# Performance work log

Measured on AMD Instinct MI355X. Metric: run time of the kernel, lower is better.

## Reference

```python
import jax, jax.numpy as jnp
import numpy as np

B, S, K = 4, 2048, 8
N_NEURONS, N_BASIS, RANK = 64, 32, 8
D_MODEL, D_HID = 256, 1024


def setup_inputs() -> dict:
    key = jax.random.key(0)
    ks = jax.random.split(key, 10)
    x = jax.random.normal(ks[0], (B, S, D_MODEL), dtype=jnp.float32)
    neuron_idx = jax.random.randint(ks[1], (B, S, K), 0, N_NEURONS)
    w = jax.random.uniform(ks[2], (B, S, K), dtype=jnp.float32)
    neuron_weights = w / jnp.sum(w, axis=-1, keepdims=True)  # softmax-like routing weights
    neuron_recipes = jax.random.normal(ks[3], (N_NEURONS, N_BASIS), dtype=jnp.float32) * 0.5
    sc = 0.1
    basis_A1 = jax.random.normal(ks[4], (N_BASIS, 16, RANK, 8), dtype=jnp.float32) * sc
    basis_A2 = jax.random.normal(ks[5], (N_BASIS, RANK, 16, 8), dtype=jnp.float32) * sc
    basis_B1 = jax.random.normal(ks[6], (N_BASIS, 8, RANK, 32), dtype=jnp.float32) * sc
    basis_B2 = jax.random.normal(ks[7], (N_BASIS, RANK, 8, 32), dtype=jnp.float32) * sc
    w_down_w = jax.random.normal(ks[8], (D_HID, D_MODEL), dtype=jnp.float32) * (1.0 / np.sqrt(D_HID))
    w_down_b = jnp.zeros((D_MODEL,), dtype=jnp.float32)
    return {
        "x": x, "neuron_idx": neuron_idx, "neuron_weights": neuron_weights,
        "neuron_recipes": neuron_recipes,
        "basis_A1": basis_A1, "basis_A2": basis_A2,
        "basis_B1": basis_B1, "basis_B2": basis_B2,
        "w_down_w": w_down_w, "w_down_b": w_down_b,
    }


def reference(x, neuron_idx, neuron_weights, neuron_recipes,
              basis_A1, basis_A2, basis_B1, basis_B2, w_down_w, w_down_b):
    Bt, St, D = x.shape
    # --- routing: gather recipes of selected neurons, softmax, weighted-combine ---
    sel = neuron_recipes[neuron_idx]                       # [B,S,k,n_basis]
    sel = jax.nn.softmax(sel, axis=-1)
    wr = jnp.einsum('bskn,bsk->bsn', sel, neuron_weights)  # [B,S,n_basis]
    # --- build per-token TT cores from basis banks (get_neuron_tt_cores) ---
    cA1 = jnp.einsum('bsn,nirk->bsirk', wr, basis_A1)      # [B,S,16,r,8]
    cA2 = jnp.einsum('bsn,nrjl->bsrjl', wr, basis_A2)      # [B,S,r,16,8]
    cB1 = jnp.einsum('bsn,nirk->bsirk', wr, basis_B1)      # [B,S,8,r,32]
    cB2 = jnp.einsum('bsn,nrjl->bsrjl', wr, basis_B2)      # [B,S,r,8,32]
    # --- TT FFN: 256 -> 64 ---
    x_fold = x.reshape(Bt, St, 16, 16)
    temp = jnp.einsum('bsij,bsirk->bsjrk', x_fold, cA1)
    h = jnp.einsum('bsjrk,bsrjl->bskl', temp, cA2).reshape(Bt, St, 64)
    # --- TT FFN: 64 -> 1024 ---
    h_fold = h.reshape(Bt, St, 8, 8)
    temp = jnp.einsum('bsij,bsirk->bsjrk', h_fold, cB1)
    out = jnp.einsum('bsjrk,bsrjl->bskl', temp, cB2).reshape(Bt, St, D_HID)
    out = jax.nn.gelu(out, approximate=False)              # torch F.gelu default = exact erf
    return out @ w_down_w + w_down_b                       # [B,S,256]
```

## Files before the change

### kernel.cpp

```cpp
#include <hip/hip_runtime.h>
#include <math.h>


typedef unsigned short u16;
typedef __attribute__((ext_vector_type(8))) __bf16 bf16x8;
typedef __attribute__((ext_vector_type(4))) float f32x4;
union ABCast { float4 f; bf16x8 v; };
union BFBits { __bf16 b; u16 u; };
union Pack8 { u16 u[8]; float4 f; };

__device__ __forceinline__ float gelu_exact(float v) {
    return 0.5f * v * (1.0f + erff(v * 0.70710678118654752440f));
}
__device__ __forceinline__ u16 f2bf_bits(float f) { BFBits c; c.b = (__bf16)f; return c.u; }
__device__ __forceinline__ float bfbits2f(u16 u) { BFBits c; c.u = u; return (float)c.b; }

__global__ __launch_bounds__(64) void k_route(
    const int* __restrict__ nidx, const float* __restrict__ nw,
    const float* __restrict__ recipes, float* __restrict__ wr_out,
    u16* __restrict__ wrAh, u16* __restrict__ wrAl)
{
    const int t = blockIdx.x * 64 + threadIdx.x;
    float acc[32];
#pragma unroll
    for (int n = 0; n < 32; n++) acc[n] = 0.f;
#pragma unroll
    for (int k = 0; k < 8; k++) {
        const int   id = nidx[t * 8 + k];
        const float wk = nw[t * 8 + k];
        const float4* row = (const float4*)(recipes + id * 32);
        float v[32];
#pragma unroll
        for (int q = 0; q < 8; q++) {
            float4 f = row[q];
            v[q*4+0] = f.x; v[q*4+1] = f.y; v[q*4+2] = f.z; v[q*4+3] = f.w;
        }
        float m = v[0];
#pragma unroll
        for (int n = 1; n < 32; n++) m = fmaxf(m, v[n]);
        float s = 0.f;
#pragma unroll
        for (int n = 0; n < 32; n++) { float e = expf(v[n] - m); v[n] = e; s += e; }
        const float iv = wk / s;
#pragma unroll
        for (int n = 0; n < 32; n++) acc[n] += v[n] * iv;
    }
    float4* o = (float4*)(wr_out + t * 32);
#pragma unroll
    for (int q = 0; q < 8; q++)
        o[q] = make_float4(acc[q*4+0], acc[q*4+1], acc[q*4+2], acc[q*4+3]);

    const int tg16 = t >> 4, tl = t & 15;
#pragma unroll
    for (int c = 0; c < 4; c++) {
        Pack8 ph, pl;
#pragma unroll
        for (int e = 0; e < 8; e++) {
            const float v = acc[c*8 + e];
            const u16 hb = f2bf_bits(v);
            ph.u[e] = hb;
            pl.u[e] = f2bf_bits(v - bfbits2f(hb));
        }
        const int lane = c * 16 + tl;
        *(float4*)(wrAh + (tg16*64 + lane)*8) = ph.f;
        *(float4*)(wrAl + (tg16*64 + lane)*8) = pl.f;
    }
}

__global__ __launch_bounds__(512) void k_stageA(
    const float* __restrict__ x, const float* __restrict__ wr,
    const float* __restrict__ A1, const float* __restrict__ A2,
    float* __restrict__ h_out)
{
    __shared__ float ca[8 * 1024];
    __shared__ float tl[8 * 1088];
    const int tid = threadIdx.x;
    const int t0  = blockIdx.x * 8;
    {
        const int e2 = tid * 2;
        float2 c[8];
#pragma unroll
        for (int tt = 0; tt < 8; tt++) c[tt] = make_float2(0.f, 0.f);
#pragma unroll 4
        for (int n = 0; n < 32; n++) {
            const float2 a = *(const float2*)(A1 + n * 1024 + e2);
#pragma unroll
            for (int tt = 0; tt < 8; tt++) {
                const float s = wr[(t0 + tt) * 32 + n];
                c[tt].x += s * a.x; c[tt].y += s * a.y;
            }
        }
#pragma unroll
        for (int tt = 0; tt < 8; tt++) *(float2*)(ca + tt * 1024 + e2) = c[tt];
    }
    __syncthreads();
    {
        const int t = tid >> 6, g = tid & 63, j = g >> 2, eh = g & 3;
        float xr[16];
#pragma unroll
        for (int i = 0; i < 16; i++) xr[i] = x[(t0 + t) * 256 + i * 16 + j];
        float tr[16];
#pragma unroll
        for (int q = 0; q < 16; q++) tr[q] = 0.f;
#pragma unroll
        for (int i = 0; i < 16; i++) {
            const float xv = xr[i];
#pragma unroll
            for (int q = 0; q < 4; q++) {
                const float4 cv = *(const float4*)(ca + t * 1024 + i * 64 + eh * 16 + q * 4);
                tr[q*4+0] += xv * cv.x; tr[q*4+1] += xv * cv.y;
                tr[q*4+2] += xv * cv.z; tr[q*4+3] += xv * cv.w;
            }
        }
#pragma unroll
        for (int q = 0; q < 4; q++)
            *(float4*)(tl + t * 1088 + j * 68 + eh * 16 + q * 4) =
                make_float4(tr[q*4+0], tr[q*4+1], tr[q*4+2], tr[q*4+3]);
    }
    __syncthreads();
    {
        const int e2 = tid * 2;
        float2 c[8];
#pragma unroll
        for (int tt = 0; tt < 8; tt++) c[tt] = make_float2(0.f, 0.f);
#pragma unroll 4
        for (int n = 0; n < 32; n++) {
            const float2 a = *(const float2*)(A2 + n * 1024 + e2);
#pragma unroll
            for (int tt = 0; tt < 8; tt++) {
                const float s = wr[(t0 + tt) * 32 + n];
                c[tt].x += s * a.x; c[tt].y += s * a.y;
            }
        }
#pragma unroll
        for (int tt = 0; tt < 8; tt++) *(float2*)(ca + tt * 1024 + e2) = c[tt];
    }
    __syncthreads();
    {
        const int t = tid >> 6, g = tid & 63, k = g >> 3, l = g & 7;
        float acc = 0.f;
#pragma unroll
        for (int j = 0; j < 16; j++) {
#pragma unroll
            for (int r = 0; r < 8; r++) {
                acc += tl[t * 1088 + j * 68 + r * 8 + k] *
                       ca[t * 1024 + r * 128 + j * 8 + l];
            }
        }
        h_out[(t0 + t) * 64 + g] = acc;
    }
}

__global__ __launch_bounds__(256) void k_bsplit(
    const float* __restrict__ B1, const float* __restrict__ B2,
    u16* __restrict__ o1h, u16* __restrict__ o1l,
    u16* __restrict__ o2h, u16* __restrict__ o2l)
{
    const int slot = blockIdx.x * 256 + threadIdx.x;
    const int bank = slot >> 13, r = (slot >> 10) & 7, g = (slot >> 6) & 15, l = slot & 63;
    const int c = l & 15, nb = 8 * (l >> 4);
    const int base = (bank == 0)
        ? ((g >> 1) * 256 + r * 32 + (g & 1) * 16 + c)
        : (r * 256 + (g >> 1) * 32 + (g & 1) * 16 + c);
    const float* S = (bank ? B2 : B1) + base + nb * 2048;
    Pack8 ph, pl;
#pragma unroll
    for (int e = 0; e < 8; e++) {
        const float v = S[e * 2048];
        const u16 hb = f2bf_bits(v);
        ph.u[e] = hb;
        pl.u[e] = f2bf_bits(v - bfbits2f(hb));
    }
    const int d = ((r * 16 + g) * 64 + l) * 8;
    *(float4*)((bank ? o2h : o1h) + d) = ph.f;
    *(float4*)((bank ? o2l : o1l) + d) = pl.f;
}

__global__ __launch_bounds__(256) void k_wsplit(
    const float* __restrict__ W, u16* __restrict__ wfh, u16* __restrict__ wfl)
{
    const int slot = blockIdx.x * 256 + threadIdx.x;
    const int ng = slot >> 11, kc = (slot >> 6) & 31, l = slot & 63;
    const float* S = W + (kc * 32 + 8 * (l >> 4)) * 256 + ng * 16 + (l & 15);
    Pack8 ph, pl;
#pragma unroll
    for (int e = 0; e < 8; e++) {
        const float v = S[e * 256];
        const u16 hb = f2bf_bits(v);
        ph.u[e] = hb;
        pl.u[e] = f2bf_bits(v - bfbits2f(hb));
    }
    const int d = ((ng * 32 + kc) * 64 + l) * 8;
    *(float4*)(wfh + d) = ph.f;
    *(float4*)(wfl + d) = pl.f;
}

__global__ __launch_bounds__(512, 2) void k_fusedB(
    const float* __restrict__ hin,
    const u16* __restrict__ wrAh, const u16* __restrict__ wrAl,
    const u16* __restrict__ bf1h, const u16* __restrict__ bf1l,
    const u16* __restrict__ bf2h, const u16* __restrict__ bf2l,
    const u16* __restrict__ wfh, const u16* __restrict__ wfl,
    const float* __restrict__ bias, float* __restrict__ y)
{
    __shared__ __align__(16) unsigned char smem[65536];
    float* hs  = (float*)smem;
    float* cb1 = hs + 1024;
    float* cb2 = cb1 + 16 * 264;
    float* t2  = cb2 + 16 * 264;
    u16* gAh = (u16*)smem;
    u16* gAl = gAh + 16384;

    const int tid = threadIdx.x;
    const int l   = tid & 63;
    const int w   = tid >> 6;
    const int tg  = blockIdx.x;
    const int t0  = tg * 16;

    {
        const float2 hv = *(const float2*)(hin + t0 * 64 + tid * 2);
        hs[tid * 2] = hv.x; hs[tid * 2 + 1] = hv.y;
    }

    ABCast cu;
    cu.f = *(const float4*)(wrAh + (tg * 64 + l) * 8); const bf16x8 wra_h = cu.v;
    cu.f = *(const float4*)(wrAl + (tg * 64 + l) * 8); const bf16x8 wra_l = cu.v;

    const bool isB2 = (w >= 4);
    const u16* bsrc_h = isB2 ? bf2h : bf1h;
    const u16* bsrc_l = isB2 ? bf2l : bf1l;
    float* cdst = isB2 ? cb2 : cb1;
    const int g0 = (w & 3) * 4;

    const int j2 = l >> 3, k42 = l & 7;
    const int k0 = (l & 7) * 4, l0 = (l >> 3) * 4;

    float o[2][4][4];
#pragma unroll
    for (int tt2 = 0; tt2 < 2; tt2++)
#pragma unroll
        for (int a = 0; a < 4; a++)
#pragma unroll
            for (int li = 0; li < 4; li++) o[tt2][a][li] = 0.f;

#pragma unroll 1
    for (int r = 0; r < 8; r++) {
#pragma unroll
        for (int gi = 0; gi < 4; gi++) {
            const int gg = g0 + gi;
            cu.f = *(const float4*)(bsrc_h + ((r*16 + gg)*64 + l)*8); const bf16x8 bh = cu.v;
            ABCast cu2;
            cu2.f = *(const float4*)(bsrc_l + ((r*16 + gg)*64 + l)*8); const bf16x8 bl = cu2.v;
            f32x4 cc = {0.f, 0.f, 0.f, 0.f};
            cc = __builtin_amdgcn_mfma_f32_16x16x32_bf16(wra_h, bh, cc, 0, 0, 0);
            cc = __builtin_amdgcn_mfma_f32_16x16x32_bf16(wra_h, bl, cc, 0, 0, 0);
            cc = __builtin_amdgcn_mfma_f32_16x16x32_bf16(wra_l, bh, cc, 0, 0, 0);
            float* cd = cdst + (gg >> 1) * 32 + (gg & 1) * 16 + (l & 15);
#pragma unroll
            for (int reg = 0; reg < 4; reg++)
                cd[(4 * (l >> 4) + reg) * 264] = cc[reg];
        }
        __syncthreads();

#pragma unroll
        for (int tt2 = 0; tt2 < 2; tt2++) {
            const int t = w + tt2 * 8;
            float4 acc = make_float4(0.f, 0.f, 0.f, 0.f);
#pragma unroll
            for (int i = 0; i < 8; i++) {
                const float  hv = hs[t * 64 + i * 8 + j2];
                const float4 cv = *(const float4*)(cb1 + t * 264 + i * 32 + k42 * 4);
                acc.x += hv * cv.x; acc.y += hv * cv.y;
                acc.z += hv * cv.z; acc.w += hv * cv.w;
            }
            *(float4*)(t2 + t * 264 + j2 * 32 + k42 * 4) = acc;
        }
        __syncthreads();

#pragma unroll
        for (int tt2 = 0; tt2 < 2; tt2++) {
            const int t = w + tt2 * 8;
#pragma unroll
            for (int j = 0; j < 8; j++) {
                const float4 tv4 = *(const float4*)(t2  + t * 264 + j * 32 + k0);
                const float4 cv4 = *(const float4*)(cb2 + t * 264 + j * 32 + l0);
                const float tv[4] = {tv4.x, tv4.y, tv4.z, tv4.w};
                const float cv[4] = {cv4.x, cv4.y, cv4.z, cv4.w};
#pragma unroll
                for (int a = 0; a < 4; a++)
#pragma unroll
                    for (int li = 0; li < 4; li++)
                        o[tt2][a][li] += tv[a] * cv[li];
            }
        }
        __syncthreads();
    }

#pragma unroll
    for (int tt2 = 0; tt2 < 2; tt2++) {
        const int t = w + tt2 * 8;
        const int lane2 = (l0 >> 3) * 16 + t;
        const int e0 = l0 & 7;
#pragma unroll
        for (int a = 0; a < 4; a++) {
            u16 hv[4], lv[4];
#pragma unroll
            for (int li = 0; li < 4; li++) {
                const float v = gelu_exact(o[tt2][a][li]);
                const u16 hb = f2bf_bits(v);
                hv[li] = hb;
                lv[li] = f2bf_bits(v - bfbits2f(hb));
            }
            const int step = k0 + a;
            *(ushort4*)(gAh + (step * 64 + lane2) * 8 + e0) = make_ushort4(hv[0], hv[1], hv[2], hv[3]);
            *(ushort4*)(gAl + (step * 64 + lane2) * 8 + e0) = make_ushort4(lv[0], lv[1], lv[2], lv[3]);
        }
    }
    __syncthreads();

    f32x4 dacc0 = {0.f, 0.f, 0.f, 0.f}, dacc1 = dacc0;
    const int wb0 = (w * 2 + 0) * 16384 + l * 8;
    const int wb1 = (w * 2 + 1) * 16384 + l * 8;
#pragma unroll 1
    for (int kc = 0; kc < 32; kc++) {
        cu.f = *(const float4*)(gAh + (kc * 64 + l) * 8); const bf16x8 ah = cu.v;
        cu.f = *(const float4*)(gAl + (kc * 64 + l) * 8); const bf16x8 al = cu.v;
        ABCast c0, c1, c2, c3;
        c0.f = *(const float4*)(wfh + wb0 + kc * 512); const bf16x8 bh0 = c0.v;
        c1.f = *(const float4*)(wfl + wb0 + kc * 512); const bf16x8 bl0 = c1.v;
        c2.f = *(const float4*)(wfh + wb1 + kc * 512); const bf16x8 bh1 = c2.v;
        c3.f = *(const float4*)(wfl + wb1 + kc * 512); const bf16x8 bl1 = c3.v;
        dacc0 = __builtin_amdgcn_mfma_f32_16x16x32_bf16(ah, bh0, dacc0, 0, 0, 0);
        dacc0 = __builtin_amdgcn_mfma_f32_16x16x32_bf16(ah, bl0, dacc0, 0, 0, 0);
        dacc0 = __builtin_amdgcn_mfma_f32_16x16x32_bf16(al, bh0, dacc0, 0, 0, 0);
        dacc1 = __builtin_amdgcn_mfma_f32_16x16x32_bf16(ah, bh1, dacc1, 0, 0, 0);
        dacc1 = __builtin_amdgcn_mfma_f32_16x16x32_bf16(ah, bl1, dacc1, 0, 0, 0);
        dacc1 = __builtin_amdgcn_mfma_f32_16x16x32_bf16(al, bh1, dacc1, 0, 0, 0);
    }
    {
        const int n0 = (w * 2 + 0) * 16 + (l & 15);
        const int n1 = (w * 2 + 1) * 16 + (l & 15);
        const float b0 = bias[n0], b1 = bias[n1];
        const int tb = t0 + 4 * (l >> 4);
#pragma unroll
        for (int reg = 0; reg < 4; reg++) {
            y[(tb + reg) * 256 + n0] = dacc0[reg] + b0;
            y[(tb + reg) * 256 + n1] = dacc1[reg] + b1;
        }
    }
}

extern "C" void kernel_launch(void* const* d_in, const int* in_sizes, int n_in,
                              void* d_out, int out_size, void* d_ws, size_t ws_size,
                              hipStream_t stream)
{
    const float* x    = (const float*)d_in[0];
    const int*   nidx = (const int*)  d_in[1];
    const float* nw   = (const float*)d_in[2];
    const float* rec  = (const float*)d_in[3];
    const float* A1   = (const float*)d_in[4];
    const float* A2   = (const float*)d_in[5];
    const float* B1   = (const float*)d_in[6];
    const float* B2   = (const float*)d_in[7];
    const float* Wd   = (const float*)d_in[8];
    const float* bd   = (const float*)d_in[9];
    float* y  = (float*)d_out;

    float* wr  = (float*)d_ws;
    float* h   = wr + 8192 * 32;
    u16* wrAh  = (u16*)(h + 8192 * 64);
    u16* wrAl  = wrAh + 262144;
    u16* b1h   = wrAl + 262144;
    u16* b1l   = b1h + 65536;
    u16* b2h   = b1l + 65536;
    u16* b2l   = b2h + 65536;
    u16* wfh   = b2l + 65536;
    u16* wfl   = wfh + 262144;

    k_route <<<128,  64,  0, stream>>>(nidx, nw, rec, wr, wrAh, wrAl);
    k_stageA<<<1024, 512, 0, stream>>>(x, wr, A1, A2, h);
    k_bsplit<<<64,   256, 0, stream>>>(B1, B2, b1h, b1l, b2h, b2l);
    k_wsplit<<<128,  256, 0, stream>>>(Wd, wfh, wfl);
    k_fusedB<<<512,  512, 0, stream>>>(h, wrAh, wrAl, b1h, b1l, b2h, b2l, wfh, wfl, bd, y);
}
```

Before: 100.1 us.

## Move per-token TT contraction in fusedB onto MFMA with pipelined core building

```diff
diff --git a/kernel.cpp b/kernel.cpp
--- a/kernel.cpp
+++ b/kernel.cpp
@@ -3,9 +3,12 @@
 
 
 typedef unsigned short u16;
+typedef unsigned int u32;
 typedef __attribute__((ext_vector_type(8))) __bf16 bf16x8;
 typedef __attribute__((ext_vector_type(4))) float f32x4;
+typedef __attribute__((ext_vector_type(16))) float f32x16;
 union ABCast { float4 f; bf16x8 v; };
+union U4Cast { u32 u[4]; bf16x8 v; };
 union BFBits { __bf16 b; u16 u; };
 union Pack8 { u16 u[8]; float4 f; };
 
@@ -204,10 +207,8 @@
     const float* __restrict__ bias, float* __restrict__ y)
 {
     __shared__ __align__(16) unsigned char smem[65536];
-    float* hs  = (float*)smem;
-    float* cb1 = hs + 1024;
-    float* cb2 = cb1 + 16 * 264;
-    float* t2  = cb2 + 16 * 264;
+    float* stg1 = (float*)smem;
+    float* stg2 = stg1 + 4096;
     u16* gAh = (u16*)smem;
     u16* gAl = gAh + 16384;
 
@@ -215,137 +216,192 @@
     const int l   = tid & 63;
     const int w   = tid >> 6;
     const int tg  = blockIdx.x;
-    const int t0  = tg * 16;
-
-    {
-        const float2 hv = *(const float2*)(hin + t0 * 64 + tid * 2);
-        hs[tid * 2] = hv.x; hs[tid * 2 + 1] = hv.y;
-    }
+    const int t0  = tg * 8;
+    const int rg16 = tg >> 1;
+    const int hb   = tg & 1;
+    const int kP  = l & 31;
+    const int jh  = l >> 5;
+
+    float hreg[32];
+#pragma unroll
+    for (int i = 0; i < 8; i++)
+#pragma unroll
+        for (int jj = 0; jj < 4; jj++)
+            hreg[i*4+jj] = hin[(t0 + w) * 64 + i * 8 + jh * 4 + jj];
 
     ABCast cu;
-    cu.f = *(const float4*)(wrAh + (tg * 64 + l) * 8); const bf16x8 wra_h = cu.v;
-    cu.f = *(const float4*)(wrAl + (tg * 64 + l) * 8); const bf16x8 wra_l = cu.v;
+    cu.f = *(const float4*)(wrAh + (rg16 * 64 + l) * 8); const bf16x8 wra_h = cu.v;
+    cu.f = *(const float4*)(wrAl + (rg16 * 64 + l) * 8); const bf16x8 wra_l = cu.v;
 
     const bool isB2 = (w >= 4);
     const u16* bsrc_h = isB2 ? bf2h : bf1h;
     const u16* bsrc_l = isB2 ? bf2l : bf1l;
-    float* cdst = isB2 ? cb2 : cb1;
+    float* cstg = isB2 ? stg2 : stg1;
     const int g0 = (w & 3) * 4;
-
-    const int j2 = l >> 3, k42 = l & 7;
-    const int k0 = (l & 7) * 4, l0 = (l >> 3) * 4;
-
-    float o[2][4][4];
-#pragma unroll
-    for (int tt2 = 0; tt2 < 2; tt2++)
-#pragma unroll
-        for (int a = 0; a < 4; a++)
-#pragma unroll
-            for (int li = 0; li < 4; li++) o[tt2][a][li] = 0.f;
+    const bool keepst = (jh == hb);
+    const int tokq = 4 * ((l >> 4) & 1);
+
+    f32x16 accw = {0.f,0.f,0.f,0.f,0.f,0.f,0.f,0.f,0.f,0.f,0.f,0.f,0.f,0.f,0.f,0.f};
+    u32 Afh0=0,Afh1=0,Afh2=0,Afh3=0, Afl0=0,Afl1=0,Afl2=0,Afl3=0;
+    u32 Bfh0=0,Bfh1=0,Bfh2=0,Bfh3=0, Bfl0=0,Bfl1=0,Bfl2=0,Bfl3=0;
+
+    float4 pA0h,pA0l,pA1h,pA1l, pB0h,pB0l,pB1h,pB1l;
+#define KLA(R) { const int rb_=(R)*16;                                          \
+    pA0h = *(const float4*)(bsrc_h + ((rb_+g0+0)*64+l)*8);                      \
+    pA0l = *(const float4*)(bsrc_l + ((rb_+g0+0)*64+l)*8);                      \
+    pA1h = *(const float4*)(bsrc_h + ((rb_+g0+1)*64+l)*8);                      \
+    pA1l = *(const float4*)(bsrc_l + ((rb_+g0+1)*64+l)*8); }
+#define KLB(R) { const int rb_=(R)*16;                                          \
+    pB0h = *(const float4*)(bsrc_h + ((rb_+g0+2)*64+l)*8);                      \
+    pB0l = *(const float4*)(bsrc_l + ((rb_+g0+2)*64+l)*8);                      \
+    pB1h = *(const float4*)(bsrc_h + ((rb_+g0+3)*64+l)*8);                      \
+    pB1l = *(const float4*)(bsrc_l + ((rb_+g0+3)*64+l)*8); }
+#define KBUILD(BSEL, G, H0, L0, H1, L1) {                                       \
+    ABCast ch_, cl_;                                                            \
+    __builtin_amdgcn_s_setprio(1);                                              \
+    ch_.f = H0; cl_.f = L0;                                                     \
+    f32x4 cc = {0.f,0.f,0.f,0.f};                                               \
+    cc = __builtin_amdgcn_mfma_f32_16x16x32_bf16(wra_h, ch_.v, cc, 0, 0, 0);    \
+    cc = __builtin_amdgcn_mfma_f32_16x16x32_bf16(wra_h, cl_.v, cc, 0, 0, 0);    \
+    cc = __builtin_amdgcn_mfma_f32_16x16x32_bf16(wra_l, ch_.v, cc, 0, 0, 0);    \
+    ch_.f = H1; cl_.f = L1;                                                     \
+    f32x4 cc2 = {0.f,0.f,0.f,0.f};                                              \
+    cc2 = __builtin_amdgcn_mfma_f32_16x16x32_bf16(wra_h, ch_.v, cc2, 0, 0, 0);  \
+    cc2 = __builtin_amdgcn_mfma_f32_16x16x32_bf16(wra_h, cl_.v, cc2, 0, 0, 0);  \
+    cc2 = __builtin_amdgcn_mfma_f32_16x16x32_bf16(wra_l, ch_.v, cc2, 0, 0, 0);  \
+    __builtin_amdgcn_s_setprio(0);                                              \
+    if (keepst) {                                                               \
+        { const int gg = (G);                                                   \
+          float* cd = cstg + (BSEL)*2048 + (gg>>1)*32 + (gg&1)*16 + (l&15);     \
+          _Pragma("unroll")                                                     \
+          for (int rg = 0; rg < 4; rg++) cd[(tokq+rg)*256] = cc[rg]; }          \
+        { const int gg = (G)+1;                                                 \
+          float* cd = cstg + (BSEL)*2048 + (gg>>1)*32 + (gg&1)*16 + (l&15);     \
+          _Pragma("unroll")                                                     \
+          for (int rg = 0; rg < 4; rg++) cd[(tokq+rg)*256] = cc2[rg]; } } }
+
+    KLA(0); KLB(0);
+    KBUILD(0, g0, pA0h, pA0l, pA1h, pA1l);
+    KBUILD(0, g0+2, pB0h, pB0l, pB1h, pB1l);
+    KLA(1); KLB(1);
+    __syncthreads();
 
 #pragma unroll 1
     for (int r = 0; r < 8; r++) {
-#pragma unroll
-        for (int gi = 0; gi < 4; gi++) {
-            const int gg = g0 + gi;
-            cu.f = *(const float4*)(bsrc_h + ((r*16 + gg)*64 + l)*8); const bf16x8 bh = cu.v;
-            ABCast cu2;
-            cu2.f = *(const float4*)(bsrc_l + ((r*16 + gg)*64 + l)*8); const bf16x8 bl = cu2.v;
-            f32x4 cc = {0.f, 0.f, 0.f, 0.f};
-            cc = __builtin_amdgcn_mfma_f32_16x16x32_bf16(wra_h, bh, cc, 0, 0, 0);
-            cc = __builtin_amdgcn_mfma_f32_16x16x32_bf16(wra_h, bl, cc, 0, 0, 0);
-            cc = __builtin_amdgcn_mfma_f32_16x16x32_bf16(wra_l, bh, cc, 0, 0, 0);
-            float* cd = cdst + (gg >> 1) * 32 + (gg & 1) * 16 + (l & 15);
-#pragma unroll
-            for (int reg = 0; reg < 4; reg++)
-                cd[(4 * (l >> 4) + reg) * 264] = cc[reg];
+        if (r < 7) {
+            KBUILD((r+1)&1, g0,   pA0h, pA0l, pA1h, pA1l);
+            KBUILD((r+1)&1, g0+2, pB0h, pB0l, pB1h, pB1l);
+            if (r < 6) { KLA(r+2); KLB(r+2); }
+        }
+
+        {
+            const float* c1b = stg1 + (r & 1) * 2048 + w * 256;
+            float t0q=0.f, t1q=0.f, t2q=0.f, t3q=0.f;
+#pragma unroll
+            for (int i = 0; i < 8; i++) {
+                const float cv = c1b[i * 32 + kP];
+                t0q += hreg[i*4+0] * cv; t1q += hreg[i*4+1] * cv;
+                t2q += hreg[i*4+2] * cv; t3q += hreg[i*4+3] * cv;
+            }
+            const u16 h0 = f2bf_bits(t0q), h1 = f2bf_bits(t1q),
+                      h2 = f2bf_bits(t2q), h3 = f2bf_bits(t3q);
+            const u16 q0 = f2bf_bits(t0q - bfbits2f(h0)), q1 = f2bf_bits(t1q - bfbits2f(h1)),
+                      q2 = f2bf_bits(t2q - bfbits2f(h2)), q3 = f2bf_bits(t3q - bfbits2f(h3));
+            const u32 th0 = (u32)h0 | ((u32)h1 << 16), th1 = (u32)h2 | ((u32)h3 << 16);
+            const u32 tl0 = (u32)q0 | ((u32)q1 << 16), tl1 = (u32)q2 | ((u32)q3 << 16);
+            const u32 ph0 = (u32)__shfl_xor((int)th0, 32);
+            const u32 ph1 = (u32)__shfl_xor((int)th1, 32);
+            const u32 pl0 = (u32)__shfl_xor((int)tl0, 32);
+            const u32 pl1 = (u32)__shfl_xor((int)tl1, 32);
+            const u32 a0 = jh ? ph0 : th0, a1 = jh ? ph1 : th1;
+            const u32 a2 = jh ? th0 : ph0, a3 = jh ? th1 : ph1;
+            const u32 b0 = jh ? pl0 : tl0, b1 = jh ? pl1 : tl1;
+            const u32 b2 = jh ? tl0 : pl0, b3 = jh ? tl1 : pl1;
+            if ((r & 1) == jh) {
+                Afh0 = a0; Afh1 = a1; Afh2 = a2; Afh3 = a3;
+                Afl0 = b0; Afl1 = b1; Afl2 = b2; Afl3 = b3;
+            }
+        }
+
+        {
+            const float* c2b = stg2 + (r & 1) * 2048 + w * 256;
+            const float v0 = c2b[0*32+kP], v1 = c2b[1*32+kP], v2 = c2b[2*32+kP],
+                        v3 = c2b[3*32+kP], v4 = c2b[4*32+kP], v5 = c2b[5*32+kP],
+                        v6 = c2b[6*32+kP], v7 = c2b[7*32+kP];
+            const u16 e0 = f2bf_bits(v0), e1 = f2bf_bits(v1), e2 = f2bf_bits(v2),
+                      e3 = f2bf_bits(v3), e4 = f2bf_bits(v4), e5 = f2bf_bits(v5),
+                      e6 = f2bf_bits(v6), e7 = f2bf_bits(v7);
+            const u16 f0 = f2bf_bits(v0 - bfbits2f(e0)), f1 = f2bf_bits(v1 - bfbits2f(e1)),
+                      f2 = f2bf_bits(v2 - bfbits2f(e2)), f3 = f2bf_bits(v3 - bfbits2f(e3)),
+                      f4 = f2bf_bits(v4 - bfbits2f(e4)), f5 = f2bf_bits(v5 - bfbits2f(e5)),
+                      f6 = f2bf_bits(v6 - bfbits2f(e6)), f7 = f2bf_bits(v7 - bfbits2f(e7));
+            if ((r & 1) == jh) {
+                Bfh0 = (u32)e0 | ((u32)e1 << 16); Bfh1 = (u32)e2 | ((u32)e3 << 16);
+                Bfh2 = (u32)e4 | ((u32)e5 << 16); Bfh3 = (u32)e6 | ((u32)e7 << 16);
+                Bfl0 = (u32)f0 | ((u32)f1 << 16); Bfl1 = (u32)f2 | ((u32)f3 << 16);
+                Bfl2 = (u32)f4 | ((u32)f5 << 16); Bfl3 = (u32)f6 | ((u32)f7 << 16);
+            }
+        }
+
+        if (r & 1) {
+            U4Cast ua;
+            ua.u[0]=Afh0; ua.u[1]=Afh1; ua.u[2]=Afh2; ua.u[3]=Afh3; const bf16x8 Ah = ua.v;
+            ua.u[0]=Afl0; ua.u[1]=Afl1; ua.u[2]=Afl2; ua.u[3]=Afl3; const bf16x8 Al = ua.v;
+            ua.u[0]=Bfh0; ua.u[1]=Bfh1; ua.u[2]=Bfh2; ua.u[3]=Bfh3; const bf16x8 Bh = ua.v;
+            ua.u[0]=Bfl0; ua.u[1]=Bfl1; ua.u[2]=Bfl2; ua.u[3]=Bfl3; const bf16x8 Bl = ua.v;
+            accw = __builtin_amdgcn_mfma_f32_32x32x16_bf16(Ah, Bh, accw, 0, 0, 0);
+            accw = __builtin_amdgcn_mfma_f32_32x32x16_bf16(Ah, Bl, accw, 0, 0, 0);
+            accw = __builtin_amdgcn_mfma_f32_32x32x16_bf16(Al, Bh, accw, 0, 0, 0);
         }
         __syncthreads();
-
-#pragma unroll
-        for (int tt2 = 0; tt2 < 2; tt2++) {
-            const int t = w + tt2 * 8;
-            float4 acc = make_float4(0.f, 0.f, 0.f, 0.f);
-#pragma unroll
-            for (int i = 0; i < 8; i++) {
-                const float  hv = hs[t * 64 + i * 8 + j2];
-                const float4 cv = *(const float4*)(cb1 + t * 264 + i * 32 + k42 * 4);
-                acc.x += hv * cv.x; acc.y += hv * cv.y;
-                acc.z += hv * cv.z; acc.w += hv * cv.w;
-            }
-            *(float4*)(t2 + t * 264 + j2 * 32 + k42 * 4) = acc;
-        }
-        __syncthreads();
-
-#pragma unroll
-        for (int tt2 = 0; tt2 < 2; tt2++) {
-            const int t = w + tt2 * 8;
-#pragma unroll
-            for (int j = 0; j < 8; j++) {
-                const float4 tv4 = *(const float4*)(t2  + t * 264 + j * 32 + k0);
-                const float4 cv4 = *(const float4*)(cb2 + t * 264 + j * 32 + l0);
-                const float tv[4] = {tv4.x, tv4.y, tv4.z, tv4.w};
-                const float cv[4] = {cv4.x, cv4.y, cv4.z, cv4.w};
-#pragma unroll
-                for (int a = 0; a < 4; a++)
-#pragma unroll
-                    for (int li = 0; li < 4; li++)
-                        o[tt2][a][li] += tv[a] * cv[li];
-            }
-        }
-        __syncthreads();
-    }
-
-#pragma unroll
-    for (int tt2 = 0; tt2 < 2; tt2++) {
-        const int t = w + tt2 * 8;
-        const int lane2 = (l0 >> 3) * 16 + t;
-        const int e0 = l0 & 7;
-#pragma unroll
-        for (int a = 0; a < 4; a++) {
-            u16 hv[4], lv[4];
-#pragma unroll
-            for (int li = 0; li < 4; li++) {
-                const float v = gelu_exact(o[tt2][a][li]);
-                const u16 hb = f2bf_bits(v);
-                hv[li] = hb;
-                lv[li] = f2bf_bits(v - bfbits2f(hb));
-            }
-            const int step = k0 + a;
-            *(ushort4*)(gAh + (step * 64 + lane2) * 8 + e0) = make_ushort4(hv[0], hv[1], hv[2], hv[3]);
-            *(ushort4*)(gAl + (step * 64 + lane2) * 8 + e0) = make_ushort4(lv[0], lv[1], lv[2], lv[3]);
+    }
+#undef KLA
+#undef KLB
+#undef KBUILD
+
+    {
+#pragma unroll
+        for (int rg = 0; rg < 16; rg++) {
+            const int k = (rg & 3) + 8 * (rg >> 2) + 4 * jh;
+            const float v = gelu_exact(accw[rg]);
+            const u16 hbits = f2bf_bits(v);
+            const u16 lbits = f2bf_bits(v - bfbits2f(hbits));
+            const int idx = (k * 64 + (kP >> 3) * 16 + w) * 8 + (kP & 7);
+            gAh[idx] = hbits; gAl[idx] = lbits;
         }
     }
     __syncthreads();
 
-    f32x4 dacc0 = {0.f, 0.f, 0.f, 0.f}, dacc1 = dacc0;
-    const int wb0 = (w * 2 + 0) * 16384 + l * 8;
-    const int wb1 = (w * 2 + 1) * 16384 + l * 8;
-#pragma unroll 1
-    for (int kc = 0; kc < 32; kc++) {
-        cu.f = *(const float4*)(gAh + (kc * 64 + l) * 8); const bf16x8 ah = cu.v;
-        cu.f = *(const float4*)(gAl + (kc * 64 + l) * 8); const bf16x8 al = cu.v;
-        ABCast c0, c1, c2, c3;
-        c0.f = *(const float4*)(wfh + wb0 + kc * 512); const bf16x8 bh0 = c0.v;
-        c1.f = *(const float4*)(wfl + wb0 + kc * 512); const bf16x8 bl0 = c1.v;
-        c2.f = *(const float4*)(wfh + wb1 + kc * 512); const bf16x8 bh1 = c2.v;
-        c3.f = *(const float4*)(wfl + wb1 + kc * 512); const bf16x8 bl1 = c3.v;
-        dacc0 = __builtin_amdgcn_mfma_f32_16x16x32_bf16(ah, bh0, dacc0, 0, 0, 0);
-        dacc0 = __builtin_amdgcn_mfma_f32_16x16x32_bf16(ah, bl0, dacc0, 0, 0, 0);
-        dacc0 = __builtin_amdgcn_mfma_f32_16x16x32_bf16(al, bh0, dacc0, 0, 0, 0);
-        dacc1 = __builtin_amdgcn_mfma_f32_16x16x32_bf16(ah, bh1, dacc1, 0, 0, 0);
-        dacc1 = __builtin_amdgcn_mfma_f32_16x16x32_bf16(ah, bl1, dacc1, 0, 0, 0);
-        dacc1 = __builtin_amdgcn_mfma_f32_16x16x32_bf16(al, bh1, dacc1, 0, 0, 0);
-    }
-    {
-        const int n0 = (w * 2 + 0) * 16 + (l & 15);
-        const int n1 = (w * 2 + 1) * 16 + (l & 15);
-        const float b0 = bias[n0], b1 = bias[n1];
-        const int tb = t0 + 4 * (l >> 4);
-#pragma unroll
-        for (int reg = 0; reg < 4; reg++) {
-            y[(tb + reg) * 256 + n0] = dacc0[reg] + b0;
-            y[(tb + reg) * 256 + n1] = dacc1[reg] + b1;
+    {
+        f32x4 dacc0 = {0.f,0.f,0.f,0.f}, dacc1 = {0.f,0.f,0.f,0.f};
+        const int wb0 = w * 16384 + l * 8;
+        const int wb1 = (w + 8) * 16384 + l * 8;
+#pragma unroll 2
+        for (int kc = 0; kc < 32; kc++) {
+            cu.f = *(const float4*)(gAh + (kc * 64 + l) * 8); const bf16x8 ah = cu.v;
+            cu.f = *(const float4*)(gAl + (kc * 64 + l) * 8); const bf16x8 al = cu.v;
+            ABCast c0, c1, c2, c3;
+            c0.f = *(const float4*)(wfh + wb0 + kc * 512); const bf16x8 bh0 = c0.v;
+            c1.f = *(const float4*)(wfl + wb0 + kc * 512); const bf16x8 bl0 = c1.v;
+            c2.f = *(const float4*)(wfh + wb1 + kc * 512); const bf16x8 bh1 = c2.v;
+            c3.f = *(const float4*)(wfl + wb1 + kc * 512); const bf16x8 bl1 = c3.v;
+            dacc0 = __builtin_amdgcn_mfma_f32_16x16x32_bf16(ah, bh0, dacc0, 0, 0, 0);
+            dacc0 = __builtin_amdgcn_mfma_f32_16x16x32_bf16(ah, bl0, dacc0, 0, 0, 0);
+            dacc0 = __builtin_amdgcn_mfma_f32_16x16x32_bf16(al, bh0, dacc0, 0, 0, 0);
+            dacc1 = __builtin_amdgcn_mfma_f32_16x16x32_bf16(ah, bh1, dacc1, 0, 0, 0);
+            dacc1 = __builtin_amdgcn_mfma_f32_16x16x32_bf16(ah, bl1, dacc1, 0, 0, 0);
+            dacc1 = __builtin_amdgcn_mfma_f32_16x16x32_bf16(al, bh1, dacc1, 0, 0, 0);
+        }
+        if (l < 32) {
+            const int n0 = w * 16 + (l & 15);
+            const int n1 = (w + 8) * 16 + (l & 15);
+            const float b0 = bias[n0], b1 = bias[n1];
+            const int tb = t0 + 4 * (l >> 4);
+#pragma unroll
+            for (int rg = 0; rg < 4; rg++) {
+                y[(tb + rg) * 256 + n0] = dacc0[rg] + b0;
+                y[(tb + rg) * 256 + n1] = dacc1[rg] + b1;
+            }
         }
     }
 }
@@ -381,5 +437,5 @@
     k_stageA<<<1024, 512, 0, stream>>>(x, wr, A1, A2, h);
     k_bsplit<<<64,   256, 0, stream>>>(B1, B2, b1h, b1l, b2h, b2l);
     k_wsplit<<<128,  256, 0, stream>>>(Wd, wfh, wfl);
-    k_fusedB<<<512,  512, 0, stream>>>(h, wrAh, wrAl, b1h, b1l, b2h, b2l, wfh, wfl, bd, y);
-}
+    k_fusedB<<<1024, 512, 0, stream>>>(h, wrAh, wrAl, b1h, b1l, b2h, b2l, wfh, wfl, bd, y);
+}
```

Result: slower. 131.1 us (+30.9%).
